# Optimization experiments

Hardware: AMD Instinct MI355X
Metric: run time of the kernel (lower is better)

Reference implementation:

```python
import jax, jax.numpy as jnp
import numpy as np

N = 8192
IN, HID, NH, TOT = 64, 64, 4, 128
DH = TOT // NH  # 32


def setup_inputs() -> dict:
    key = jax.random.key(0)
    ks = jax.random.split(key, 8)
    s = 0.05
    return {
        "input": jax.random.normal(ks[0], (N, IN), jnp.float32),
        "hx": jax.random.normal(ks[1], (N, HID), jnp.float32),
        "Wq": jax.random.normal(ks[2], (NH, TOT, DH), jnp.float32) * s,
        "Wk": jax.random.normal(ks[3], (NH, TOT, DH), jnp.float32) * s,
        "Wr": jax.random.normal(ks[4], (TOT, HID), jnp.float32) * s,
        "br": jnp.zeros((HID,), jnp.float32),
        "Wz": jax.random.normal(ks[5], (TOT, HID), jnp.float32) * s,
        "bz": jnp.zeros((HID,), jnp.float32),
        "Wh": jax.random.normal(ks[6], (TOT, HID), jnp.float32) * s,
        "bh": jnp.zeros((HID,), jnp.float32),
    }


def _dyn_adj(x, Wq, Wk):
    # x: [N, T]; multi-head attention adjacency, averaged over heads -> [N, N]
    q = jnp.einsum('nt,htd->hnd', x, Wq)
    k = jnp.einsum('nt,htd->hnd', x, Wk)
    scores = jnp.einsum('hnd,hmd->hnm', q, k) / jnp.sqrt(jnp.float32(DH))
    return jnp.mean(jax.nn.softmax(scores, axis=-1), axis=0)  # [N, N]


def reference(input, hx, Wq, Wk, Wr, br, Wz, bz, Wh, bh):
    x = jnp.concatenate([input, hx], axis=1)          # [N, TOT]
    adj = _dyn_adj(x, Wq, Wk)                         # [N, N] row-stochastic
    ax = adj @ x                                      # shared adjacency application
    r = jax.nn.sigmoid(ax @ Wr + br)                  # [N, HID]
    z = jax.nn.sigmoid(ax @ Wz + bz)                  # [N, HID]
    x2 = jnp.concatenate([input, r * hx], axis=1)     # [N, TOT]
    h = jnp.tanh((adj @ x2) @ Wh + bh)                # [N, HID]
    return z * hx + (1.0 - z) * h
```

## Files before the change

### kernel.cpp

```cpp
#include <hip/hip_runtime.h>
#include <hip/hip_bf16.h>

#define NN 8192
#define TOTD 128
#define HIDD 64
#define NHEAD 4
#define DHD 32
#define NCQ 16
#define JPB (NN / 32 / NCQ)

typedef __attribute__((ext_vector_type(8))) short short8;
typedef __attribute__((ext_vector_type(4))) float f32x4;
typedef __attribute__((ext_vector_type(16))) float f32x16;

__device__ __forceinline__ short f2b(float f) {
  unsigned u = __builtin_bit_cast(unsigned, f);
  u += 0x7fff + ((u >> 16) & 1);
  return (short)(u >> 16);
}
__device__ __forceinline__ short f2b_fast(float f) {
  unsigned u = __builtin_bit_cast(unsigned, f);
  return (short)((u + 0x8000u) >> 16);
}
__device__ __forceinline__ float fexp2(float x) {
#if __has_builtin(__builtin_amdgcn_exp2f)
  return __builtin_amdgcn_exp2f(x);
#else
  return exp2f(x);
#endif
}
__device__ __forceinline__ f32x16 zero16() {
  f32x16 z;
#pragma unroll
  for (int i = 0; i < 16; ++i) z[i] = 0.f;
  return z;
}


__global__ void k_build_xfrag(const float* __restrict__ in, const float* __restrict__ hx,
                              short* __restrict__ xb) {
  int i = blockIdx.x * 256 + threadIdx.x;
  int n = i >> 7;
  int t = i & 127;
  float v = (t < 64) ? in[n * 64 + t] : hx[n * 64 + (t - 64)];
  int jt = n >> 5, nn = n & 31;
  int m = nn >> 4, rem = nn & 15;
  int hi = (rem >> 2) & 1;
  int e = (rem & 3) | ((rem >> 3) << 2);
  int ct = t >> 5;
  int lane = (hi << 5) | (t & 31);
  xb[(((size_t)jt * 8 + ct * 2 + m) << 9) + (lane << 3) + e] = f2b(v);
}

__global__ __launch_bounds__(256, 2) void k_qk(
    const float* __restrict__ in, const float* __restrict__ hx,
    const float* __restrict__ Wq, const float* __restrict__ Wk,
    short* __restrict__ qb, short* __restrict__ kb) {
  __shared__ float Ws[32 * 256];
  __shared__ float xr_t[128 * 16];
  const int tid = threadIdx.x;
  const int n0 = blockIdx.x * 16;
  for (int i = tid; i < 2048; i += 256) {
    int r = i & 15, t = i >> 4;
    xr_t[t * 16 + r] = (t < 64) ? in[(n0 + r) * 64 + t] : hx[(n0 + r) * 64 + (t - 64)];
  }
  const int which = tid >> 7;
  const int h = (tid >> 5) & 3;
  const int d = tid & 31;
  const int c = tid;
  float acc[16];
#pragma unroll
  for (int r = 0; r < 16; ++r) acc[r] = 0.f;

  for (int pass = 0; pass < 4; ++pass) {
    __syncthreads();
    for (int i = tid; i < 32 * 256; i += 256) {
      int tt = pass * 32 + (i >> 8);
      int cc = i & 255;
      const float* W = (cc < 128) ? Wq : Wk;
      int hh = (cc >> 5) & 3, dd = cc & 31;
      Ws[(i >> 8) * 256 + cc] = W[((size_t)hh * 128 + tt) * 32 + dd];
    }
    __syncthreads();
#pragma unroll
    for (int t = 0; t < 32; ++t) {
      float wv = Ws[t * 256 + c];
      const float4* xp = (const float4*)&xr_t[(pass * 32 + t) * 16];
      float4 x0 = xp[0], x1 = xp[1], x2 = xp[2], x3 = xp[3];
      acc[0] += x0.x * wv;  acc[1] += x0.y * wv;  acc[2] += x0.z * wv;  acc[3] += x0.w * wv;
      acc[4] += x1.x * wv;  acc[5] += x1.y * wv;  acc[6] += x1.z * wv;  acc[7] += x1.w * wv;
      acc[8] += x2.x * wv;  acc[9] += x2.y * wv;  acc[10] += x2.z * wv; acc[11] += x2.w * wv;
      acc[12] += x3.x * wv; acc[13] += x3.y * wv; acc[14] += x3.z * wv; acc[15] += x3.w * wv;
    }
  }
#pragma unroll
  for (int r = 0; r < 16; ++r) {
    int n = n0 + r;
    int lane = (((d >> 3) & 1) << 5) | (n & 31);
    size_t idx = ((((size_t)(n >> 5) * 4 + h) * 2 + (d >> 4)) << 9) + (lane << 3) + (d & 7);
    if (which == 0) qb[idx] = f2b(acc[r] * 0.25503486f);
    else            kb[idx] = f2b(acc[r]);
  }
}

__global__ __launch_bounds__(256, 4) void k_denom(
    const short* __restrict__ qb, const short* __restrict__ kb,
    float* __restrict__ lpart_g) {
  const int tid = threadIdx.x;
  const int w = tid >> 6, l = tid & 63;
  const int r0 = blockIdx.x * 128 + w * 32;
  const int rt = blockIdx.x * 4 + w;
  const int jt0 = blockIdx.y * JPB;

  short8 qf[NHEAD][2];
#pragma unroll
  for (int h = 0; h < NHEAD; ++h)
#pragma unroll
    for (int m = 0; m < 2; ++m)
      qf[h][m] = *(const short8*)&qb[((((size_t)rt * 4 + h) * 2 + m) << 9) + l * 8];

  float acc[NHEAD] = {0.f, 0.f, 0.f, 0.f};

  for (int j = 0; j < JPB; ++j) {
    const short* kbase = kb + (((size_t)(jt0 + j) * 8) << 9) + l * 8;
#pragma unroll
    for (int h = 0; h < NHEAD; ++h) {
      short8 kf0 = *(const short8*)&kbase[(h * 2 + 0) << 9];
      short8 kf1 = *(const short8*)&kbase[(h * 2 + 1) << 9];
      f32x16 s = __builtin_amdgcn_mfma_f32_32x32x16_bf16(kf0, qf[h][0], zero16(), 0, 0, 0);
      s = __builtin_amdgcn_mfma_f32_32x32x16_bf16(kf1, qf[h][1], s, 0, 0, 0);
#pragma unroll
      for (int r = 0; r < 16; ++r) acc[h] += fexp2(s[r]);
    }
  }
#pragma unroll
  for (int h = 0; h < NHEAD; ++h) acc[h] += __shfl_xor(acc[h], 32, 64);
  if (l < 32) {
#pragma unroll
    for (int h = 0; h < NHEAD; ++h)
      lpart_g[((size_t)blockIdx.y * NHEAD + h) * NN + r0 + l] = acc[h];
  }
}

__global__ void k_linv(const float* __restrict__ lpart_g, float* __restrict__ linv_g) {
  int i = blockIdx.x * 256 + threadIdx.x;
  float s = 0.f;
#pragma unroll
  for (int q = 0; q < NCQ; ++q) s += lpart_g[(size_t)q * NHEAD * NN + i];
  linv_g[i] = 0.25f / s;
}

__global__ __launch_bounds__(256, 2) void k_pv1(
    const short* __restrict__ qb, const short* __restrict__ kb,
    const short* __restrict__ xb, const float* __restrict__ linv_g,
    float* __restrict__ axq) {
  const int tid = threadIdx.x;
  const int w = tid >> 6, l = tid & 63;
  const int hi = l >> 5, col = l & 31;
  const int r0 = blockIdx.x * 128 + w * 32;
  const int rt = blockIdx.x * 4 + w;
  const int jt0 = blockIdx.y * JPB;

  short8 qf[NHEAD][2];
#pragma unroll
  for (int h = 0; h < NHEAD; ++h)
#pragma unroll
    for (int m = 0; m < 2; ++m)
      qf[h][m] = *(const short8*)&qb[((((size_t)rt * 4 + h) * 2 + m) << 9) + l * 8];
  float linv[NHEAD];
#pragma unroll
  for (int h = 0; h < NHEAD; ++h) linv[h] = linv_g[h * NN + r0 + col];

  f32x16 axa[4];
#pragma unroll
  for (int ct = 0; ct < 4; ++ct) axa[ct] = zero16();

  for (int j = 0; j < JPB; ++j) {
    const size_t jt = jt0 + j;
    const short* kbase = kb + ((jt * 8) << 9) + l * 8;
    const short* xbase = xb + ((jt * 8) << 9) + l * 8;
    short8 xv[8];
#pragma unroll
    for (int cchunk = 0; cchunk < 8; ++cchunk)
      xv[cchunk] = *(const short8*)&xbase[cchunk << 9];
    float p[16];
#pragma unroll
    for (int r = 0; r < 16; ++r) p[r] = 0.f;
#pragma unroll
    for (int h = 0; h < NHEAD; ++h) {
      short8 kf0 = *(const short8*)&kbase[(h * 2 + 0) << 9];
      short8 kf1 = *(const short8*)&kbase[(h * 2 + 1) << 9];
      f32x16 s = __builtin_amdgcn_mfma_f32_32x32x16_bf16(kf0, qf[h][0], zero16(), 0, 0, 0);
      s = __builtin_amdgcn_mfma_f32_32x32x16_bf16(kf1, qf[h][1], s, 0, 0, 0);
#pragma unroll
      for (int r = 0; r < 16; ++r) p[r] += fexp2(s[r]) * linv[h];
    }
    short8 pa0, pa1;
#pragma unroll
    for (int e = 0; e < 8; ++e) { pa0[e] = f2b_fast(p[e]); pa1[e] = f2b_fast(p[8 + e]); }
#pragma unroll
    for (int ct = 0; ct < 4; ++ct) {
      axa[ct] = __builtin_amdgcn_mfma_f32_32x32x16_bf16(pa0, xv[ct * 2 + 0], axa[ct], 0, 0, 0);
      axa[ct] = __builtin_amdgcn_mfma_f32_32x32x16_bf16(pa1, xv[ct * 2 + 1], axa[ct], 0, 0, 0);
    }
  }
#pragma unroll
  for (int ct = 0; ct < 4; ++ct)
#pragma unroll
    for (int r = 0; r < 16; ++r) {
      int row = (r & 3) + 8 * (r >> 2) + 4 * hi;
      axq[(size_t)blockIdx.y * NN * TOTD + (size_t)(r0 + row) * TOTD + ct * 32 + col] =
          axa[ct][r];
    }
}

__global__ void k_rz(const float* __restrict__ axq, const float* __restrict__ hx,
                     const float* __restrict__ Wr, const float* __restrict__ br,
                     const float* __restrict__ Wz, const float* __restrict__ bz,
                     float* __restrict__ ax, float* __restrict__ z,
                     short* __restrict__ v2f) {
  __shared__ float axs[2][TOTD];
  int tid = threadIdx.x;
  int rr = tid >> 7;
  int c2 = tid & 127;
  int n = blockIdx.x * 2 + rr;
  float s = 0.f;
#pragma unroll
  for (int q = 0; q < NCQ; ++q) s += axq[(size_t)q * NN * TOTD + (size_t)n * TOTD + c2];
  axs[rr][c2] = s;
  ax[(size_t)n * TOTD + c2] = s;
  __syncthreads();
  bool isz = c2 >= HIDD;
  int c = c2 & (HIDD - 1);
  const float* W = isz ? Wz : Wr;
  float acc = isz ? bz[c] : br[c];
#pragma unroll
  for (int t = 0; t < TOTD; ++t) acc += axs[rr][t] * W[t * HIDD + c];
  float sg = 1.f / (1.f + __expf(-acc));
  if (isz) {
    z[n * HIDD + c] = sg;
  } else {
    int jt = n >> 5, nn = n & 31;
    int m = nn >> 4, rem = nn & 15;
    int hi = (rem >> 2) & 1;
    int e = (rem & 3) | ((rem >> 3) << 2);
    int ct = c >> 5;
    int lane = (hi << 5) | (c & 31);
    v2f[(((size_t)jt * 4 + ct * 2 + m) << 9) + (lane << 3) + e] = f2b(sg * hx[n * HIDD + c]);
  }
}

__global__ __launch_bounds__(256, 3) void k_pv2(
    const short* __restrict__ qb, const short* __restrict__ kb,
    const short* __restrict__ v2f, const float* __restrict__ linv_g,
    float* __restrict__ a2q) {
  const int tid = threadIdx.x;
  const int w = tid >> 6, l = tid & 63;
  const int hi = l >> 5, col = l & 31;
  const int r0 = blockIdx.x * 128 + w * 32;
  const int rt = blockIdx.x * 4 + w;
  const int jt0 = blockIdx.y * JPB;

  short8 qf[NHEAD][2];
#pragma unroll
  for (int h = 0; h < NHEAD; ++h)
#pragma unroll
    for (int m = 0; m < 2; ++m)
      qf[h][m] = *(const short8*)&qb[((((size_t)rt * 4 + h) * 2 + m) << 9) + l * 8];
  float linv[NHEAD];
#pragma unroll
  for (int h = 0; h < NHEAD; ++h) linv[h] = linv_g[h * NN + r0 + col];

  f32x16 a2a[2];
#pragma unroll
  for (int ct = 0; ct < 2; ++ct) a2a[ct] = zero16();

  for (int j = 0; j < JPB; ++j) {
    const size_t jt = jt0 + j;
    const short* kbase = kb + ((jt * 8) << 9) + l * 8;
    const short* vbase = v2f + ((jt * 4) << 9) + l * 8;
    short8 vv[4];
#pragma unroll
    for (int cchunk = 0; cchunk < 4; ++cchunk)
      vv[cchunk] = *(const short8*)&vbase[cchunk << 9];
    float p[16];
#pragma unroll
    for (int r = 0; r < 16; ++r) p[r] = 0.f;
#pragma unroll
    for (int h = 0; h < NHEAD; ++h) {
      short8 kf0 = *(const short8*)&kbase[(h * 2 + 0) << 9];
      short8 kf1 = *(const short8*)&kbase[(h * 2 + 1) << 9];
      f32x16 s = __builtin_amdgcn_mfma_f32_32x32x16_bf16(kf0, qf[h][0], zero16(), 0, 0, 0);
      s = __builtin_amdgcn_mfma_f32_32x32x16_bf16(kf1, qf[h][1], s, 0, 0, 0);
#pragma unroll
      for (int r = 0; r < 16; ++r) p[r] += fexp2(s[r]) * linv[h];
    }
    short8 pa0, pa1;
#pragma unroll
    for (int e = 0; e < 8; ++e) { pa0[e] = f2b_fast(p[e]); pa1[e] = f2b_fast(p[8 + e]); }
#pragma unroll
    for (int ct = 0; ct < 2; ++ct) {
      a2a[ct] = __builtin_amdgcn_mfma_f32_32x32x16_bf16(pa0, vv[ct * 2 + 0], a2a[ct], 0, 0, 0);
      a2a[ct] = __builtin_amdgcn_mfma_f32_32x32x16_bf16(pa1, vv[ct * 2 + 1], a2a[ct], 0, 0, 0);
    }
  }
#pragma unroll
  for (int ct = 0; ct < 2; ++ct)
#pragma unroll
    for (int r = 0; r < 16; ++r) {
      int row = (r & 3) + 8 * (r >> 2) + 4 * hi;
      a2q[(size_t)blockIdx.y * NN * HIDD + (size_t)(r0 + row) * HIDD + ct * 32 + col] =
          a2a[ct][r];
    }
}

__global__ __launch_bounds__(256) void k_final(
    const float* __restrict__ a2q, const float* __restrict__ ax,
    const float* __restrict__ hx, const float* __restrict__ Wh,
    const float* __restrict__ bh, const float* __restrict__ z,
    float* __restrict__ out) {
  __shared__ float Whs[TOTD * HIDD];
  __shared__ float a2s[16][HIDD];
  const int tid = threadIdx.x;
  const int r0 = blockIdx.x * 16;

  for (int i = tid; i < TOTD * HIDD; i += 256) Whs[i] = Wh[i];
  for (int i = tid; i < 16 * HIDD; i += 256) {
    int rw = i >> 6, c = i & 63;
    size_t gi = (size_t)(r0 + rw) * HIDD + c;
    float s = 0.f;
#pragma unroll
    for (int q = 0; q < NCQ; ++q) s += a2q[(size_t)q * NN * HIDD + gi];
    a2s[rw][c] = s;
  }
  __syncthreads();
  for (int o = tid; o < 16 * HIDD; o += 256) {
    int rw = o >> 6, c = o & 63;
    const float* axrow = &ax[(size_t)(r0 + rw) * TOTD];
    float acc = bh[c];
#pragma unroll
    for (int t = 0; t < 64; ++t) acc += axrow[t] * Whs[t * HIDD + c];
#pragma unroll
    for (int t = 0; t < 64; ++t) acc += a2s[rw][t] * Whs[(64 + t) * HIDD + c];
    float hval = tanhf(acc);
    size_t gi = (size_t)(r0 + rw) * HIDD + c;
    float zz = z[gi];
    out[gi] = zz * hx[gi] + (1.f - zz) * hval;
  }
}

extern "C" void kernel_launch(void* const* d_in, const int* in_sizes, int n_in,
                              void* d_out, int out_size, void* d_ws, size_t ws_size,
                              hipStream_t stream) {
  const float* in = (const float*)d_in[0];
  const float* hx = (const float*)d_in[1];
  const float* Wq = (const float*)d_in[2];
  const float* Wk = (const float*)d_in[3];
  const float* Wr = (const float*)d_in[4];
  const float* br = (const float*)d_in[5];
  const float* Wz = (const float*)d_in[6];
  const float* bz = (const float*)d_in[7];
  const float* Wh = (const float*)d_in[8];
  const float* bh = (const float*)d_in[9];

  const size_t MB = 1ull << 20;
  char* ws = (char*)d_ws;
  short* qb    = (short*)(ws + 0 * MB);
  short* kb    = (short*)(ws + 2 * MB);
  short* xb    = (short*)(ws + 4 * MB);
  float* linv  = (float*)(ws + 6 * MB);
  float* lpart = (float*)(ws + 7 * MB);
  float* ax    = (float*)(ws + 10 * MB);
  float* z     = (float*)(ws + 14 * MB);
  short* v2f   = (short*)(ws + 16 * MB);
  float* axq   = (float*)(ws + 20 * MB);
  float* a2q   = (float*)(ws + 84 * MB);
  float* out   = (float*)d_out;

  k_build_xfrag<<<dim3((NN * TOTD) / 256), dim3(256), 0, stream>>>(in, hx, xb);
  k_qk<<<dim3(NN / 16), dim3(256), 0, stream>>>(in, hx, Wq, Wk, qb, kb);
  k_denom<<<dim3(NN / 128, NCQ), dim3(256), 0, stream>>>(qb, kb, lpart);
  k_linv<<<dim3((NHEAD * NN) / 256), dim3(256), 0, stream>>>(lpart, linv);
  k_pv1<<<dim3(NN / 128, NCQ), dim3(256), 0, stream>>>(qb, kb, xb, linv, axq);
  k_rz<<<dim3(NN / 2), dim3(256), 0, stream>>>(axq, hx, Wr, br, Wz, bz, ax, z, v2f);
  k_pv2<<<dim3(NN / 128, NCQ), dim3(256), 0, stream>>>(qb, kb, v2f, linv, a2q);
  k_final<<<dim3(NN / 16), dim3(256), 0, stream>>>(a2q, ax, hx, Wh, bh, z, out);
}
```

Measured before the change: 210.0 us.

## Cache bf16 attention matrix from first pass and reuse it in second pass

```diff
diff --git a/kernel.cpp b/kernel.cpp
--- a/kernel.cpp
+++ b/kernel.cpp
@@ -21,6 +21,10 @@
 __device__ __forceinline__ short f2b_fast(float f) {
   unsigned u = __builtin_bit_cast(unsigned, f);
   return (short)((u + 0x8000u) >> 16);
+}
+__device__ __forceinline__ float b2f(short s) {
+  unsigned u = ((unsigned)(unsigned short)s) << 16;
+  return __builtin_bit_cast(float, u);
 }
 __device__ __forceinline__ float fexp2(float x) {
 #if __has_builtin(__builtin_amdgcn_exp2f)
@@ -153,7 +157,7 @@
 __global__ __launch_bounds__(256, 2) void k_pv1(
     const short* __restrict__ qb, const short* __restrict__ kb,
     const short* __restrict__ xb, const float* __restrict__ linv_g,
-    float* __restrict__ axq) {
+    short* __restrict__ axq, short* __restrict__ Pf, int storeP) {
   const int tid = threadIdx.x;
   const int w = tid >> 6, l = tid & 63;
   const int hi = l >> 5, col = l & 31;
@@ -198,6 +202,11 @@
     short8 pa0, pa1;
 #pragma unroll
     for (int e = 0; e < 8; ++e) { pa0[e] = f2b_fast(p[e]); pa1[e] = f2b_fast(p[8 + e]); }
+    if (storeP) {
+      short8* pdst = (short8*)&Pf[(((size_t)rt * 256 + jt) << 10) + (l << 4)];
+      pdst[0] = pa0;
+      pdst[1] = pa1;
+    }
 #pragma unroll
     for (int ct = 0; ct < 4; ++ct) {
       axa[ct] = __builtin_amdgcn_mfma_f32_32x32x16_bf16(pa0, xv[ct * 2 + 0], axa[ct], 0, 0, 0);
@@ -210,50 +219,65 @@
     for (int r = 0; r < 16; ++r) {
       int row = (r & 3) + 8 * (r >> 2) + 4 * hi;
       axq[(size_t)blockIdx.y * NN * TOTD + (size_t)(r0 + row) * TOTD + ct * 32 + col] =
-          axa[ct][r];
-    }
-}
-
-__global__ void k_rz(const float* __restrict__ axq, const float* __restrict__ hx,
-                     const float* __restrict__ Wr, const float* __restrict__ br,
-                     const float* __restrict__ Wz, const float* __restrict__ bz,
-                     float* __restrict__ ax, float* __restrict__ z,
-                     short* __restrict__ v2f) {
-  __shared__ float axs[2][TOTD];
-  int tid = threadIdx.x;
-  int rr = tid >> 7;
-  int c2 = tid & 127;
-  int n = blockIdx.x * 2 + rr;
-  float s = 0.f;
-#pragma unroll
-  for (int q = 0; q < NCQ; ++q) s += axq[(size_t)q * NN * TOTD + (size_t)n * TOTD + c2];
-  axs[rr][c2] = s;
-  ax[(size_t)n * TOTD + c2] = s;
+          f2b(axa[ct][r]);
+    }
+}
+
+__global__ __launch_bounds__(256) void k_rz(
+    const short* __restrict__ axq, const float* __restrict__ hx,
+    const float* __restrict__ Wr, const float* __restrict__ br,
+    const float* __restrict__ Wz, const float* __restrict__ bz,
+    float* __restrict__ ax, float* __restrict__ z, short* __restrict__ v2f) {
+  __shared__ float axs[8][TOTD];
+  const int tid = threadIdx.x;
+  const int n0 = blockIdx.x * 8;
+  for (int i = tid; i < 8 * TOTD; i += 256) {
+    int rw = i >> 7, c = i & 127;
+    int n = n0 + rw;
+    float s = 0.f;
+#pragma unroll
+    for (int q = 0; q < NCQ; ++q) s += b2f(axq[((size_t)q * NN + n) * TOTD + c]);
+    axs[rw][c] = s;
+    if (c < 64) ax[(size_t)n * HIDD + c] = s;
+  }
   __syncthreads();
-  bool isz = c2 >= HIDD;
-  int c = c2 & (HIDD - 1);
+  const int c2 = tid & 127;
+  const int half = tid >> 7;
+  const bool isz = c2 >= HIDD;
+  const int c = c2 & (HIDD - 1);
   const float* W = isz ? Wz : Wr;
-  float acc = isz ? bz[c] : br[c];
-#pragma unroll
-  for (int t = 0; t < TOTD; ++t) acc += axs[rr][t] * W[t * HIDD + c];
-  float sg = 1.f / (1.f + __expf(-acc));
-  if (isz) {
-    z[n * HIDD + c] = sg;
-  } else {
-    int jt = n >> 5, nn = n & 31;
-    int m = nn >> 4, rem = nn & 15;
-    int hi = (rem >> 2) & 1;
-    int e = (rem & 3) | ((rem >> 3) << 2);
-    int ct = c >> 5;
-    int lane = (hi << 5) | (c & 31);
-    v2f[(((size_t)jt * 4 + ct * 2 + m) << 9) + (lane << 3) + e] = f2b(sg * hx[n * HIDD + c]);
-  }
-}
-
-__global__ __launch_bounds__(256, 3) void k_pv2(
-    const short* __restrict__ qb, const short* __restrict__ kb,
-    const short* __restrict__ v2f, const float* __restrict__ linv_g,
-    float* __restrict__ a2q) {
+  const float bias = isz ? bz[c] : br[c];
+  float a0 = bias, a1 = bias, a2 = bias, a3 = bias;
+#pragma unroll
+  for (int t = 0; t < TOTD; ++t) {
+    float wv = W[t * HIDD + c];
+    a0 += axs[half * 4 + 0][t] * wv;
+    a1 += axs[half * 4 + 1][t] * wv;
+    a2 += axs[half * 4 + 2][t] * wv;
+    a3 += axs[half * 4 + 3][t] * wv;
+  }
+  float accs[4] = {a0, a1, a2, a3};
+#pragma unroll
+  for (int r = 0; r < 4; ++r) {
+    int n = n0 + half * 4 + r;
+    float sg = 1.f / (1.f + __expf(-accs[r]));
+    if (isz) {
+      z[(size_t)n * HIDD + c] = sg;
+    } else {
+      int jt = n >> 5, nn = n & 31;
+      int m = nn >> 4, rem = nn & 15;
+      int hh = (rem >> 2) & 1;
+      int e = (rem & 3) | ((rem >> 3) << 2);
+      int ct = c >> 5;
+      int lane = (hh << 5) | (c & 31);
+      v2f[(((size_t)jt * 4 + ct * 2 + m) << 9) + (lane << 3) + e] = f2b(sg * hx[(size_t)n * HIDD + c]);
+    }
+  }
+}
+
+__global__ __launch_bounds__(256, 8) void k_pv2P(
+    const short* __restrict__ Pf, const short* __restrict__ v2f,
+    short* __restrict__ a2q) {
   const int tid = threadIdx.x;
   const int w = tid >> 6, l = tid & 63;
   const int hi = l >> 5, col = l & 31;
@@ -261,6 +285,46 @@
   const int rt = blockIdx.x * 4 + w;
   const int jt0 = blockIdx.y * JPB;
 
+  f32x16 a2a[2];
+#pragma unroll
+  for (int ct = 0; ct < 2; ++ct) a2a[ct] = zero16();
+
+  for (int j = 0; j < JPB; ++j) {
+    const size_t jt = jt0 + j;
+    const short8* pbase = (const short8*)&Pf[(((size_t)rt * 256 + jt) << 10) + (l << 4)];
+    short8 pa0 = pbase[0];
+    short8 pa1 = pbase[1];
+    const short* vbase = v2f + ((jt * 4) << 9) + l * 8;
+    short8 vv0 = *(const short8*)&vbase[0 << 9];
+    short8 vv1 = *(const short8*)&vbase[1 << 9];
+    short8 vv2 = *(const short8*)&vbase[2 << 9];
+    short8 vv3 = *(const short8*)&vbase[3 << 9];
+    a2a[0] = __builtin_amdgcn_mfma_f32_32x32x16_bf16(pa0, vv0, a2a[0], 0, 0, 0);
+    a2a[0] = __builtin_amdgcn_mfma_f32_32x32x16_bf16(pa1, vv1, a2a[0], 0, 0, 0);
+    a2a[1] = __builtin_amdgcn_mfma_f32_32x32x16_bf16(pa0, vv2, a2a[1], 0, 0, 0);
+    a2a[1] = __builtin_amdgcn_mfma_f32_32x32x16_bf16(pa1, vv3, a2a[1], 0, 0, 0);
+  }
+#pragma unroll
+  for (int ct = 0; ct < 2; ++ct)
+#pragma unroll
+    for (int r = 0; r < 16; ++r) {
+      int row = (r & 3) + 8 * (r >> 2) + 4 * hi;
+      a2q[(size_t)blockIdx.y * NN * HIDD + (size_t)(r0 + row) * HIDD + ct * 32 + col] =
+          f2b(a2a[ct][r]);
+    }
+}
+
+__global__ __launch_bounds__(256, 3) void k_pv2R(
+    const short* __restrict__ qb, const short* __restrict__ kb,
+    const short* __restrict__ v2f, const float* __restrict__ linv_g,
+    short* __restrict__ a2q) {
+  const int tid = threadIdx.x;
+  const int w = tid >> 6, l = tid & 63;
+  const int hi = l >> 5, col = l & 31;
+  const int r0 = blockIdx.x * 128 + w * 32;
+  const int rt = blockIdx.x * 4 + w;
+  const int jt0 = blockIdx.y * JPB;
+
   short8 qf[NHEAD][2];
 #pragma unroll
   for (int h = 0; h < NHEAD; ++h)
@@ -279,10 +343,10 @@
     const size_t jt = jt0 + j;
     const short* kbase = kb + ((jt * 8) << 9) + l * 8;
     const short* vbase = v2f + ((jt * 4) << 9) + l * 8;
-    short8 vv[4];
-#pragma unroll
-    for (int cchunk = 0; cchunk < 4; ++cchunk)
-      vv[cchunk] = *(const short8*)&vbase[cchunk << 9];
+    short8 vv0 = *(const short8*)&vbase[0 << 9];
+    short8 vv1 = *(const short8*)&vbase[1 << 9];
+    short8 vv2 = *(const short8*)&vbase[2 << 9];
+    short8 vv3 = *(const short8*)&vbase[3 << 9];
     float p[16];
 #pragma unroll
     for (int r = 0; r < 16; ++r) p[r] = 0.f;
@@ -298,11 +362,10 @@
     short8 pa0, pa1;
 #pragma unroll
     for (int e = 0; e < 8; ++e) { pa0[e] = f2b_fast(p[e]); pa1[e] = f2b_fast(p[8 + e]); }
-#pragma unroll
-    for (int ct = 0; ct < 2; ++ct) {
-      a2a[ct] = __builtin_amdgcn_mfma_f32_32x32x16_bf16(pa0, vv[ct * 2 + 0], a2a[ct], 0, 0, 0);
-      a2a[ct] = __builtin_amdgcn_mfma_f32_32x32x16_bf16(pa1, vv[ct * 2 + 1], a2a[ct], 0, 0, 0);
-    }
+    a2a[0] = __builtin_amdgcn_mfma_f32_32x32x16_bf16(pa0, vv0, a2a[0], 0, 0, 0);
+    a2a[0] = __builtin_amdgcn_mfma_f32_32x32x16_bf16(pa1, vv1, a2a[0], 0, 0, 0);
+    a2a[1] = __builtin_amdgcn_mfma_f32_32x32x16_bf16(pa0, vv2, a2a[1], 0, 0, 0);
+    a2a[1] = __builtin_amdgcn_mfma_f32_32x32x16_bf16(pa1, vv3, a2a[1], 0, 0, 0);
   }
 #pragma unroll
   for (int ct = 0; ct < 2; ++ct)
@@ -310,12 +373,12 @@
     for (int r = 0; r < 16; ++r) {
       int row = (r & 3) + 8 * (r >> 2) + 4 * hi;
       a2q[(size_t)blockIdx.y * NN * HIDD + (size_t)(r0 + row) * HIDD + ct * 32 + col] =
-          a2a[ct][r];
+          f2b(a2a[ct][r]);
     }
 }
 
 __global__ __launch_bounds__(256) void k_final(
-    const float* __restrict__ a2q, const float* __restrict__ ax,
+    const short* __restrict__ a2q, const float* __restrict__ ax,
     const float* __restrict__ hx, const float* __restrict__ Wh,
     const float* __restrict__ bh, const float* __restrict__ z,
     float* __restrict__ out) {
@@ -330,13 +393,13 @@
     size_t gi = (size_t)(r0 + rw) * HIDD + c;
     float s = 0.f;
 #pragma unroll
-    for (int q = 0; q < NCQ; ++q) s += a2q[(size_t)q * NN * HIDD + gi];
+    for (int q = 0; q < NCQ; ++q) s += b2f(a2q[(size_t)q * NN * HIDD + gi]);
     a2s[rw][c] = s;
   }
   __syncthreads();
   for (int o = tid; o < 16 * HIDD; o += 256) {
     int rw = o >> 6, c = o & 63;
-    const float* axrow = &ax[(size_t)(r0 + rw) * TOTD];
+    const float* axrow = &ax[(size_t)(r0 + rw) * HIDD];
     float acc = bh[c];
 #pragma unroll
     for (int t = 0; t < 64; ++t) acc += axrow[t] * Whs[t * HIDD + c];
@@ -369,20 +432,25 @@
   short* kb    = (short*)(ws + 2 * MB);
   short* xb    = (short*)(ws + 4 * MB);
   float* linv  = (float*)(ws + 6 * MB);
-  float* lpart = (float*)(ws + 7 * MB);
-  float* ax    = (float*)(ws + 10 * MB);
-  float* z     = (float*)(ws + 14 * MB);
-  short* v2f   = (short*)(ws + 16 * MB);
-  float* axq   = (float*)(ws + 20 * MB);
-  float* a2q   = (float*)(ws + 84 * MB);
+  float* lpart = (float*)(ws + 6 * MB + 524288);
+  float* ax    = (float*)(ws + 7 * MB);
+  float* z     = (float*)(ws + 9 * MB);
+  short* v2f   = (short*)(ws + 11 * MB);
+  short* axq   = (short*)(ws + 12 * MB);
+  short* a2q   = (short*)(ws + 44 * MB);
+  short* Pf    = (short*)(ws + 60 * MB);
   float* out   = (float*)d_out;
+  int useP = (ws_size >= 188 * MB) ? 1 : 0;
 
   k_build_xfrag<<<dim3((NN * TOTD) / 256), dim3(256), 0, stream>>>(in, hx, xb);
   k_qk<<<dim3(NN / 16), dim3(256), 0, stream>>>(in, hx, Wq, Wk, qb, kb);
   k_denom<<<dim3(NN / 128, NCQ), dim3(256), 0, stream>>>(qb, kb, lpart);
   k_linv<<<dim3((NHEAD * NN) / 256), dim3(256), 0, stream>>>(lpart, linv);
-  k_pv1<<<dim3(NN / 128, NCQ), dim3(256), 0, stream>>>(qb, kb, xb, linv, axq);
-  k_rz<<<dim3(NN / 2), dim3(256), 0, stream>>>(axq, hx, Wr, br, Wz, bz, ax, z, v2f);
-  k_pv2<<<dim3(NN / 128, NCQ), dim3(256), 0, stream>>>(qb, kb, v2f, linv, a2q);
+  k_pv1<<<dim3(NN / 128, NCQ), dim3(256), 0, stream>>>(qb, kb, xb, linv, axq, Pf, useP);
+  k_rz<<<dim3(NN / 8), dim3(256), 0, stream>>>(axq, hx, Wr, br, Wz, bz, ax, z, v2f);
+  if (useP)
+    k_pv2P<<<dim3(NN / 128, NCQ), dim3(256), 0, stream>>>(Pf, v2f, a2q);
+  else
+    k_pv2R<<<dim3(NN / 128, NCQ), dim3(256), 0, stream>>>(qb, kb, v2f, linv, a2q);
   k_final<<<dim3(NN / 16), dim3(256), 0, stream>>>(a2q, ax, hx, Wh, bh, z, out);
 }
```

Result: faster. 205.4 us (-2.2%).
